# Kernel optimization log

Hardware: AMD Instinct MI355X
Metric: run time of the kernel (lower is better)

## Reference

```python
import jax, jax.numpy as jnp
import numpy as np

DIM = 1024
N_HEADS = 16
HEAD_DIM = DIM // N_HEADS


def setup_inputs() -> dict:
    key = jax.random.key(0)
    ks = jax.random.split(key, 5)
    scale = 1.0 / np.sqrt(DIM)
    x = jax.random.normal(ks[0], (2, 2048, DIM), dtype=jnp.float32)
    W_qkv = jax.random.normal(ks[1], (DIM, 3 * DIM), dtype=jnp.float32) * scale
    b_qkv = jax.random.normal(ks[2], (3 * DIM,), dtype=jnp.float32) * 0.01
    W_proj = jax.random.normal(ks[3], (DIM, DIM), dtype=jnp.float32) * scale
    b_proj = jax.random.normal(ks[4], (DIM,), dtype=jnp.float32) * 0.01
    return {"x": x, "W_qkv": W_qkv, "b_qkv": b_qkv, "W_proj": W_proj, "b_proj": b_proj}


def reference(x, W_qkv, b_qkv, W_proj, b_proj):
    B, T, C = x.shape
    qkv = x @ W_qkv + b_qkv  # [B,T,3C]
    q, k, v = jnp.split(qkv, 3, axis=2)
    # [B,T,C] -> [B,H,T,Dh]
    def heads(y):
        return y.reshape(B, T, N_HEADS, HEAD_DIM).transpose(0, 2, 1, 3)
    q, k, v = heads(q), heads(k), heads(v)
    inv_sqrt_dh = 1.0 / jnp.sqrt(jnp.asarray(HEAD_DIM, dtype=x.dtype))
    attn = jnp.einsum('bhqd,bhkd->bhqk', q, k) * inv_sqrt_dh
    attn = jax.nn.softmax(attn, axis=-1)
    out = jnp.einsum('bhqk,bhkd->bhqd', attn, v)
    out = out.transpose(0, 2, 1, 3).reshape(B, T, C)
    return out @ W_proj + b_proj
```

## Files before the change

kernel.cpp:

```cpp
#include <hip/hip_runtime.h>
#include <hip/hip_bf16.h>
#include <math.h>

using bf16 = __hip_bfloat16;

typedef __bf16 bf16x8 __attribute__((ext_vector_type(8)));
typedef __bf16 bf16x4 __attribute__((ext_vector_type(4)));
typedef float  f32x4  __attribute__((ext_vector_type(4)));
typedef float  f32x16 __attribute__((ext_vector_type(16)));

constexpr int Bb = 2;
constexpr int Ts = 2048;
constexpr int Cc = 1024;
constexpr int Hh = 16;
constexpr int Dh = 64;
constexpr int Mm = Bb * Ts;
constexpr int Nqkv = 3 * Cc;
constexpr int BHTD = Bb * Hh * Ts * Dh;

__device__ __forceinline__
void gll16(const __bf16* g, __bf16* l)
{
    __builtin_amdgcn_global_load_lds(
        (const __attribute__((address_space(1))) unsigned int*)g,
        (__attribute__((address_space(3))) unsigned int*)l,
        16, 0, 0);
}

__global__ __launch_bounds__(256)
void prep_all(const float* __restrict__ x, __bf16* __restrict__ Xb,
              const float* __restrict__ Wq, __bf16* __restrict__ Wqt,
              const float* __restrict__ Wp, __bf16* __restrict__ Wpt)
{
    __shared__ __bf16 tl[64][72];
    const int bid = blockIdx.x;
    const int t = threadIdx.x;

    if (bid < 4096) {
        int i = (bid * 256 + t) * 4;
        float4 v = *(const float4*)(x + i);
        bf16x4 o = { (__bf16)v.x, (__bf16)v.y, (__bf16)v.z, (__bf16)v.w };
        *(bf16x4*)(Xb + i) = o;
        return;
    }
    const float* W; __bf16* Wt; int cols, bx, by;
    if (bid < 4096 + 768) {
        W = Wq; Wt = Wqt; cols = Nqkv;
        bx = (bid - 4096) % 48; by = (bid - 4096) / 48;
    } else {
        W = Wp; Wt = Wpt; cols = Cc;
        bx = (bid - 4864) % 16; by = (bid - 4864) / 16;
    }
    const int c0 = bx * 64;
    const int r0 = by * 64;
    #pragma unroll
    for (int i = 0; i < 4; i++) {
        int e = t + 256 * i;
        int r = e >> 4, c4 = (e & 15) * 4;
        float4 v = *(const float4*)(W + (r0 + r) * cols + c0 + c4);
        bf16x4 o = { (__bf16)v.x, (__bf16)v.y, (__bf16)v.z, (__bf16)v.w };
        *(bf16x4*)&tl[r][c4] = o;
    }
    __syncthreads();
    #pragma unroll
    for (int i = 0; i < 4; i++) {
        int e = t + 256 * i;
        int n = e >> 4, k4 = (e & 15) * 4;
        bf16x4 o = { tl[k4][n], tl[k4 + 1][n], tl[k4 + 2][n], tl[k4 + 3][n] };
        *(bf16x4*)(Wt + (c0 + n) * 1024 + r0 + k4) = o;
    }
}

__device__ __forceinline__
void gemm_core(const __bf16* __restrict__ A, const __bf16* __restrict__ Bt,
               int m0, int n0, int wm, int wn, int quad, int l16, int t,
               f32x4 (&acc)[4][4])
{
    __shared__ __bf16 Al[128][32];
    __shared__ __bf16 Bl[128][32];

    const int wave = t >> 6;
    const int lane = t & 63;
    const int srow = lane >> 2;
    const int scol = (lane & 3) * 8;

    const __bf16* Ag = A  + (size_t)(m0 + wave * 16 + srow) * 1024 + scol;
    const __bf16* Bg = Bt + (size_t)(n0 + wave * 16 + srow) * 1024 + scol;
    __bf16* Al_lo = &Al[wave * 16][0];
    __bf16* Al_hi = &Al[64 + wave * 16][0];
    __bf16* Bl_lo = &Bl[wave * 16][0];
    __bf16* Bl_hi = &Bl[64 + wave * 16][0];

    for (int k0 = 0; k0 < 1024; k0 += 32) {
        gll16(Ag + k0,             Al_lo);
        gll16(Ag + k0 + 64 * 1024, Al_hi);
        gll16(Bg + k0,             Bl_lo);
        gll16(Bg + k0 + 64 * 1024, Bl_hi);
        __syncthreads();
        bf16x8 af[4], bfr[4];
        #pragma unroll
        for (int mt = 0; mt < 4; mt++)
            af[mt] = *(const bf16x8*)&Al[wm * 64 + mt * 16 + l16][quad * 8];
        #pragma unroll
        for (int nt = 0; nt < 4; nt++)
            bfr[nt] = *(const bf16x8*)&Bl[wn * 64 + nt * 16 + l16][quad * 8];
        #pragma unroll
        for (int mt = 0; mt < 4; mt++)
            #pragma unroll
            for (int nt = 0; nt < 4; nt++)
                acc[mt][nt] = __builtin_amdgcn_mfma_f32_16x16x32_bf16(
                    af[mt], bfr[nt], acc[mt][nt], 0, 0, 0);
        __syncthreads();
    }
}

__global__ __launch_bounds__(256)
void qkv_mfma(const __bf16* __restrict__ A, const __bf16* __restrict__ Bt,
              const float* __restrict__ bias, __bf16* __restrict__ qkv)
{
    __shared__ __bf16 ebuf[4][64][72];

    const int t    = threadIdx.x;
    const int wave = t >> 6;
    const int lane = t & 63;
    const int quad = lane >> 4;
    const int l16  = lane & 15;
    const int wm   = wave >> 1, wn = wave & 1;
    const int n0 = blockIdx.x * 128;
    const int m0 = blockIdx.y * 128;

    f32x4 acc[4][4];
    #pragma unroll
    for (int i = 0; i < 4; i++)
        #pragma unroll
        for (int j = 0; j < 4; j++)
            acc[i][j] = f32x4{0.f, 0.f, 0.f, 0.f};

    gemm_core(A, Bt, m0, n0, wm, wn, quad, l16, t, acc);

    const int nw0 = n0 + wn * 64;
    const int which = nw0 >> 10;
    const int h = (nw0 & 1023) >> 6;

    if (which == 2) {
        #pragma unroll
        for (int nt = 0; nt < 4; nt++) {
            int d = nt * 16 + l16;
            float bs = bias[nw0 + nt * 16 + l16];
            #pragma unroll
            for (int mt = 0; mt < 4; mt++) {
                int m = m0 + wm * 64 + mt * 16 + quad * 4;
                int b = m >> 11;
                int tt = m & 2047;
                bf16x4 o = { (__bf16)(acc[mt][nt][0] + bs),
                             (__bf16)(acc[mt][nt][1] + bs),
                             (__bf16)(acc[mt][nt][2] + bs),
                             (__bf16)(acc[mt][nt][3] + bs) };
                *(bf16x4*)&qkv[2 * (size_t)BHTD +
                               (((size_t)(b * 16 + h) * 64 + d) * 2048 + tt)] = o;
            }
        }
    } else {
        #pragma unroll
        for (int nt = 0; nt < 4; nt++) {
            float bs = bias[nw0 + nt * 16 + l16];
            #pragma unroll
            for (int mt = 0; mt < 4; mt++)
                #pragma unroll
                for (int r = 0; r < 4; r++)
                    ebuf[wave][mt * 16 + quad * 4 + r][nt * 16 + l16] =
                        (__bf16)(acc[mt][nt][r] + bs);
        }
        int m = m0 + wm * 64 + lane;
        int b = m >> 11;
        int tt = m & 2047;
        __bf16* dst = &qkv[which * (size_t)BHTD +
                           (((size_t)(b * 16 + h) * 2048 + tt) * 64)];
        #pragma unroll
        for (int c = 0; c < 8; c++)
            *(bf16x8*)(dst + c * 8) = *(const bf16x8*)&ebuf[wave][lane][c * 8];
    }
}

__global__ __launch_bounds__(256)
void proj_mfma(const __bf16* __restrict__ A, const __bf16* __restrict__ Bt,
               const float* __restrict__ bias, float* __restrict__ out)
{
    const int t    = threadIdx.x;
    const int wave = t >> 6;
    const int lane = t & 63;
    const int quad = lane >> 4;
    const int l16  = lane & 15;
    const int wm   = wave >> 1, wn = wave & 1;
    const int n0 = blockIdx.x * 128;
    const int m0 = blockIdx.y * 128;

    f32x4 acc[4][4];
    #pragma unroll
    for (int i = 0; i < 4; i++)
        #pragma unroll
        for (int j = 0; j < 4; j++)
            acc[i][j] = f32x4{0.f, 0.f, 0.f, 0.f};

    gemm_core(A, Bt, m0, n0, wm, wn, quad, l16, t, acc);

    #pragma unroll
    for (int nt = 0; nt < 4; nt++) {
        int n = n0 + wn * 64 + nt * 16 + l16;
        float bs = bias[n];
        #pragma unroll
        for (int mt = 0; mt < 4; mt++) {
            #pragma unroll
            for (int r = 0; r < 4; r++) {
                int m = m0 + wm * 64 + mt * 16 + quad * 4 + r;
                out[m * 1024 + n] = acc[mt][nt][r] + bs;
            }
        }
    }
}

__global__ __launch_bounds__(512, 2)
void attn_mfma(const __bf16* __restrict__ Q, const __bf16* __restrict__ K,
               const __bf16* __restrict__ VT, __bf16* __restrict__ O)
{
    __shared__ __bf16 sK[2][3][64 * 64];
    __shared__ __bf16 sV[2][3][64 * 64];
    __shared__ float  slsum[4][2][64];

    const int t    = threadIdx.x;
    const int wave = t >> 6;
    const int lane = t & 63;
    const int qg   = wave & 3;
    const int kh   = wave >> 2;
    const int c    = lane & 31;
    const int hi   = lane >> 5;
    const int hx   = hi * 16;
    const int sw   = (c & 7) << 4;

    const int blk = blockIdx.x;
    const int bh  = blk & 31;
    const int qc  = blk >> 5;
    const int q0  = qc * 256 + qg * 64;

    const __bf16* Qp = Q  + ((size_t)bh * Ts + q0) * Dh;
    const __bf16* Kp = K  + (size_t)bh * Ts * Dh;
    const __bf16* Vp = VT + (size_t)bh * Dh * Ts;

    const float qscale = 0.125f * 1.44269504088896f;
    bf16x8 qf[2][4];
    #pragma unroll
    for (int qs = 0; qs < 2; qs++)
        #pragma unroll
        for (int ds = 0; ds < 4; ds++) {
            bf16x8 v = *(const bf16x8*)(Qp + (qs * 32 + c) * Dh + ds * 16 + hi * 8);
            #pragma unroll
            for (int i = 0; i < 8; i++) v[i] = (__bf16)(qscale * (float)v[i]);
            qf[qs][ds] = v;
        }

    f32x16 accO[2][2];
    #pragma unroll
    for (int qs = 0; qs < 2; qs++)
        #pragma unroll
        for (int dt = 0; dt < 2; dt++)
            #pragma unroll
            for (int i = 0; i < 16; i++) accO[qs][dt][i] = 0.f;
    float lsum[2] = {0.f, 0.f};

    const f32x16 z16 = {0.f, 0.f, 0.f, 0.f, 0.f, 0.f, 0.f, 0.f,
                        0.f, 0.f, 0.f, 0.f, 0.f, 0.f, 0.f, 0.f};

    const int r0 = qg * 8 + (lane >> 3);
    const int s8 = ((lane & 7) ^ (r0 & 7)) * 8;
    const __bf16* kg0 = Kp + (size_t)(kh * 1024 + r0) * Dh + s8;
    const __bf16* kg1 = kg0 + 32 * Dh;
    const __bf16* vg0 = Vp + (size_t)r0 * Ts + kh * 1024 + s8;
    const __bf16* vg1 = vg0 + (size_t)32 * Ts;

    gll16(kg0, &sK[kh][0][qg * 512]);
    gll16(kg1, &sK[kh][0][2048 + qg * 512]);
    gll16(vg0, &sV[kh][0][qg * 512]);
    gll16(vg1, &sV[kh][0][2048 + qg * 512]);

    for (int j = 0; j < 16; j++) {
        const int p = j % 3;
        if (j < 15) {
            const int pn = (j + 1) % 3;
            gll16(kg0 + (j + 1) * 4096, &sK[kh][pn][qg * 512]);
            gll16(kg1 + (j + 1) * 4096, &sK[kh][pn][2048 + qg * 512]);
            gll16(vg0 + (j + 1) * 64,   &sV[kh][pn][qg * 512]);
            gll16(vg1 + (j + 1) * 64,   &sV[kh][pn][2048 + qg * 512]);
            asm volatile("s_waitcnt vmcnt(4)" ::: "memory");
        } else {
            asm volatile("s_waitcnt vmcnt(0)" ::: "memory");
        }
        __builtin_amdgcn_s_barrier();
        __builtin_amdgcn_sched_barrier(0);

        const char* kb = (const char*)&sK[kh][p][0];
        const char* vb = (const char*)&sV[kh][p][0];

        bf16x8 kf[2][4];
        #pragma unroll
        for (int kt = 0; kt < 2; kt++) {
            const char* rbase = kb + (kt * 32 + c) * 128;
            #pragma unroll
            for (int ds = 0; ds < 4; ds++)
                kf[kt][ds] = *(const bf16x8*)(rbase + ((ds * 32 + hx) ^ sw));
        }

        f32x16 st[2][2];
        __builtin_amdgcn_s_setprio(1);
        #pragma unroll
        for (int kt = 0; kt < 2; kt++)
            #pragma unroll
            for (int qs = 0; qs < 2; qs++)
                st[qs][kt] = __builtin_amdgcn_mfma_f32_32x32x16_bf16(
                    kf[kt][0], qf[qs][0], z16, 0, 0, 0);
        #pragma unroll
        for (int ds = 1; ds < 4; ds++)
            #pragma unroll
            for (int kt = 0; kt < 2; kt++)
                #pragma unroll
                for (int qs = 0; qs < 2; qs++)
                    st[qs][kt] = __builtin_amdgcn_mfma_f32_32x32x16_bf16(
                        kf[kt][ds], qf[qs][ds], st[qs][kt], 0, 0, 0);
        __builtin_amdgcn_s_setprio(0);

        bf16x8 pa[2][4];
        #pragma unroll
        for (int qs = 0; qs < 2; qs++) {
            unsigned pk[2][8];
            #pragma unroll
            for (int kt = 0; kt < 2; kt++) {
                float sum0 = 0.f, sum1 = 0.f;
                #pragma unroll
                for (int r = 0; r < 16; r++) {
                    float pv = __builtin_amdgcn_exp2f(st[qs][kt][r]);
                    st[qs][kt][r] = pv;
                    if (r & 1) sum1 += pv; else sum0 += pv;
                }
                lsum[qs] += sum0 + sum1;
                #pragma unroll
                for (int r2 = 0; r2 < 8; r2++) {
                    unsigned d;
                    asm("v_cvt_pk_bf16_f32 %0, %1, %2"
                        : "=v"(d)
                        : "v"(st[qs][kt][2 * r2]), "v"(st[qs][kt][2 * r2 + 1]));
                    pk[kt][r2] = d;
                }
            }
            #pragma unroll
            for (int s = 0; s < 4; s++) {
                const int kt = s >> 1, r4 = (s & 1) * 4;
                unsigned x0 = pk[kt][r4 + 0], y0 = pk[kt][r4 + 2];
                unsigned x1 = pk[kt][r4 + 1], y1 = pk[kt][r4 + 3];
                asm("v_permlane32_swap_b32 %0, %1" : "+v"(x0), "+v"(y0));
                asm("v_permlane32_swap_b32 %0, %1" : "+v"(x1), "+v"(y1));
                union { unsigned u[4]; bf16x8 b; } pu;
                pu.u[0] = x0; pu.u[1] = x1; pu.u[2] = y0; pu.u[3] = y1;
                pa[qs][s] = pu.b;
            }
        }

        __builtin_amdgcn_s_setprio(1);
        #pragma unroll
        for (int s = 0; s < 4; s++)
            #pragma unroll
            for (int dt = 0; dt < 2; dt++) {
                bf16x8 vf = *(const bf16x8*)(vb + (dt * 32 + c) * 128 +
                                             ((s * 32 + hx) ^ sw));
                #pragma unroll
                for (int qs = 0; qs < 2; qs++)
                    accO[qs][dt] = __builtin_amdgcn_mfma_f32_32x32x16_bf16(
                        pa[qs][s], vf, accO[qs][dt], 0, 0, 0);
            }
        __builtin_amdgcn_s_setprio(0);
    }

    __syncthreads();

    float* pb = (qg < 2) ? (float*)&sK[0][0][0] + qg * 4096
                         : (float*)&sV[0][0][0] + (qg - 2) * 4096;
    if (kh == 1) {
        #pragma unroll
        for (int qs = 0; qs < 2; qs++) {
            #pragma unroll
            for (int dt = 0; dt < 2; dt++)
                #pragma unroll
                for (int r = 0; r < 16; r++)
                    pb[((qs * 2 + dt) << 10) + (r << 6) + lane] = accO[qs][dt][r];
            slsum[qg][qs][lane] = lsum[qs];
        }
    }
    __syncthreads();
    if (kh == 0) {
        #pragma unroll
        for (int qs = 0; qs < 2; qs++) {
            #pragma unroll
            for (int dt = 0; dt < 2; dt++)
                #pragma unroll
                for (int r = 0; r < 16; r++)
                    accO[qs][dt][r] += pb[((qs * 2 + dt) << 10) + (r << 6) + lane];
            lsum[qs] += slsum[qg][qs][lane];
        }

        const int b = bh >> 4, h = bh & 15;
        #pragma unroll
        for (int qs = 0; qs < 2; qs++) {
            float l = lsum[qs] + __shfl_xor(lsum[qs], 32);
            float linv = 1.f / l;
            #pragma unroll
            for (int r = 0; r < 16; r++) {
                const int qrow = (r & 3) + 8 * (r >> 2) + 4 * hi;
                float inv = __shfl(linv, qrow);
                __bf16* Op = O + ((size_t)(b * Ts + q0 + qs * 32 + qrow)) * Cc +
                             h * 64 + c;
                Op[0]  = (__bf16)(accO[qs][0][r] * inv);
                Op[32] = (__bf16)(accO[qs][1][r] * inv);
            }
        }
    }
}

extern "C" void kernel_launch(void* const* d_in, const int* in_sizes, int n_in,
                              void* d_out, int out_size, void* d_ws, size_t ws_size,
                              hipStream_t stream)
{
    (void)in_sizes; (void)n_in; (void)out_size; (void)ws_size;
    const float* x     = (const float*)d_in[0];
    const float* Wqkv  = (const float*)d_in[1];
    const float* bqkv  = (const float*)d_in[2];
    const float* Wproj = (const float*)d_in[3];
    const float* bproj = (const float*)d_in[4];
    float* out = (float*)d_out;

    __bf16* ws   = (__bf16*)d_ws;
    __bf16* Qw   = ws;
    __bf16* XbAO = ws + 3 * (size_t)BHTD;
    __bf16* Wqt  = XbAO + (size_t)Mm * Cc;
    __bf16* Wpt  = Wqt + (size_t)Nqkv * Cc;

    prep_all<<<dim3(5120), 256, 0, stream>>>(x, XbAO, Wqkv, Wqt, Wproj, Wpt);
    qkv_mfma<<<dim3(Nqkv / 128, Mm / 128), 256, 0, stream>>>(XbAO, Wqt, bqkv, Qw);
    attn_mfma<<<dim3(256), 512, 0, stream>>>(
        Qw, Qw + BHTD, Qw + 2 * (size_t)BHTD, XbAO);
    proj_mfma<<<dim3(Cc / 128, Mm / 128), 256, 0, stream>>>(XbAO, Wpt, bproj, out);
}
```

Before: 189.1 us.

## Halve attention and projection tiles to double block counts and occupancy

The attention kernel now gives each wave 32 query rows instead of 64 and launches 512 blocks instead of 256. It drops from triple to double buffering of K/V in shared memory and fuses the score, exp and PV steps per 32-key subtile, which cuts register and LDS use so four blocks can fit per CU. The projection GEMM switches to 64-row M tiles through a templated gemm_core, doubling its grid to fill more CUs. In exchange, K/V tiles are reloaded twice as often per query, and the double buffer leaves less prefetch slack because of the full vmcnt(0) wait at the top of each iteration.

```diff
diff --git a/kernel.cpp b/kernel.cpp
--- a/kernel.cpp
+++ b/kernel.cpp
@@ -71,14 +71,16 @@
     }
 }
 
+template<int BM>
 __device__ __forceinline__
 void gemm_core(const __bf16* __restrict__ A, const __bf16* __restrict__ Bt,
                int m0, int n0, int wm, int wn, int quad, int l16, int t,
                f32x4 (&acc)[4][4])
 {
-    __shared__ __bf16 Al[128][32];
+    __shared__ __bf16 Al[BM][32];
     __shared__ __bf16 Bl[128][32];
 
+    constexpr int MT = BM / 32;
     const int wave = t >> 6;
     const int lane = t & 63;
     const int srow = lane >> 2;
@@ -87,25 +89,27 @@
     const __bf16* Ag = A  + (size_t)(m0 + wave * 16 + srow) * 1024 + scol;
     const __bf16* Bg = Bt + (size_t)(n0 + wave * 16 + srow) * 1024 + scol;
     __bf16* Al_lo = &Al[wave * 16][0];
-    __bf16* Al_hi = &Al[64 + wave * 16][0];
     __bf16* Bl_lo = &Bl[wave * 16][0];
     __bf16* Bl_hi = &Bl[64 + wave * 16][0];
 
     for (int k0 = 0; k0 < 1024; k0 += 32) {
-        gll16(Ag + k0,             Al_lo);
-        gll16(Ag + k0 + 64 * 1024, Al_hi);
+        gll16(Ag + k0, Al_lo);
+        if constexpr (BM == 128) {
+            __bf16* Al_hi = &Al[64 + wave * 16][0];
+            gll16(Ag + k0 + 64 * 1024, Al_hi);
+        }
         gll16(Bg + k0,             Bl_lo);
         gll16(Bg + k0 + 64 * 1024, Bl_hi);
         __syncthreads();
-        bf16x8 af[4], bfr[4];
-        #pragma unroll
-        for (int mt = 0; mt < 4; mt++)
-            af[mt] = *(const bf16x8*)&Al[wm * 64 + mt * 16 + l16][quad * 8];
+        bf16x8 af[MT], bfr[4];
+        #pragma unroll
+        for (int mt = 0; mt < MT; mt++)
+            af[mt] = *(const bf16x8*)&Al[wm * (BM / 2) + mt * 16 + l16][quad * 8];
         #pragma unroll
         for (int nt = 0; nt < 4; nt++)
             bfr[nt] = *(const bf16x8*)&Bl[wn * 64 + nt * 16 + l16][quad * 8];
         #pragma unroll
-        for (int mt = 0; mt < 4; mt++)
+        for (int mt = 0; mt < MT; mt++)
             #pragma unroll
             for (int nt = 0; nt < 4; nt++)
                 acc[mt][nt] = __builtin_amdgcn_mfma_f32_16x16x32_bf16(
@@ -136,7 +140,7 @@
         for (int j = 0; j < 4; j++)
             acc[i][j] = f32x4{0.f, 0.f, 0.f, 0.f};
 
-    gemm_core(A, Bt, m0, n0, wm, wn, quad, l16, t, acc);
+    gemm_core<128>(A, Bt, m0, n0, wm, wn, quad, l16, t, acc);
 
     const int nw0 = n0 + wn * 64;
     const int which = nw0 >> 10;
@@ -193,7 +197,7 @@
     const int l16  = lane & 15;
     const int wm   = wave >> 1, wn = wave & 1;
     const int n0 = blockIdx.x * 128;
-    const int m0 = blockIdx.y * 128;
+    const int m0 = blockIdx.y * 64;
 
     f32x4 acc[4][4];
     #pragma unroll
@@ -202,30 +206,30 @@
         for (int j = 0; j < 4; j++)
             acc[i][j] = f32x4{0.f, 0.f, 0.f, 0.f};
 
-    gemm_core(A, Bt, m0, n0, wm, wn, quad, l16, t, acc);
+    gemm_core<64>(A, Bt, m0, n0, wm, wn, quad, l16, t, acc);
 
     #pragma unroll
     for (int nt = 0; nt < 4; nt++) {
         int n = n0 + wn * 64 + nt * 16 + l16;
         float bs = bias[n];
         #pragma unroll
-        for (int mt = 0; mt < 4; mt++) {
+        for (int mt = 0; mt < 2; mt++) {
             #pragma unroll
             for (int r = 0; r < 4; r++) {
-                int m = m0 + wm * 64 + mt * 16 + quad * 4 + r;
+                int m = m0 + wm * 32 + mt * 16 + quad * 4 + r;
                 out[m * 1024 + n] = acc[mt][nt][r] + bs;
             }
         }
     }
 }
 
-__global__ __launch_bounds__(512, 2)
+__global__ __launch_bounds__(512, 4)
 void attn_mfma(const __bf16* __restrict__ Q, const __bf16* __restrict__ K,
                const __bf16* __restrict__ VT, __bf16* __restrict__ O)
 {
-    __shared__ __bf16 sK[2][3][64 * 64];
-    __shared__ __bf16 sV[2][3][64 * 64];
-    __shared__ float  slsum[4][2][64];
+    __shared__ __bf16 sK[2][2][64 * 64];
+    __shared__ __bf16 sV[2][2][64 * 64];
+    __shared__ float  slsum[4][64];
 
     const int t    = threadIdx.x;
     const int wave = t >> 6;
@@ -240,32 +244,28 @@
     const int blk = blockIdx.x;
     const int bh  = blk & 31;
     const int qc  = blk >> 5;
-    const int q0  = qc * 256 + qg * 64;
+    const int q0  = qc * 128 + qg * 32;
 
     const __bf16* Qp = Q  + ((size_t)bh * Ts + q0) * Dh;
     const __bf16* Kp = K  + (size_t)bh * Ts * Dh;
     const __bf16* Vp = VT + (size_t)bh * Dh * Ts;
 
     const float qscale = 0.125f * 1.44269504088896f;
-    bf16x8 qf[2][4];
-    #pragma unroll
-    for (int qs = 0; qs < 2; qs++)
-        #pragma unroll
-        for (int ds = 0; ds < 4; ds++) {
-            bf16x8 v = *(const bf16x8*)(Qp + (qs * 32 + c) * Dh + ds * 16 + hi * 8);
-            #pragma unroll
-            for (int i = 0; i < 8; i++) v[i] = (__bf16)(qscale * (float)v[i]);
-            qf[qs][ds] = v;
-        }
-
-    f32x16 accO[2][2];
-    #pragma unroll
-    for (int qs = 0; qs < 2; qs++)
-        #pragma unroll
-        for (int dt = 0; dt < 2; dt++)
-            #pragma unroll
-            for (int i = 0; i < 16; i++) accO[qs][dt][i] = 0.f;
-    float lsum[2] = {0.f, 0.f};
+    bf16x8 qf[4];
+    #pragma unroll
+    for (int ds = 0; ds < 4; ds++) {
+        bf16x8 v = *(const bf16x8*)(Qp + c * Dh + ds * 16 + hi * 8);
+        #pragma unroll
+        for (int i = 0; i < 8; i++) v[i] = (__bf16)(qscale * (float)v[i]);
+        qf[ds] = v;
+    }
+
+    f32x16 accO[2];
+    #pragma unroll
+    for (int dt = 0; dt < 2; dt++)
+        #pragma unroll
+        for (int i = 0; i < 16; i++) accO[dt][i] = 0.f;
+    float lsum = 0.f;
 
     const f32x16 z16 = {0.f, 0.f, 0.f, 0.f, 0.f, 0.f, 0.f, 0.f,
                         0.f, 0.f, 0.f, 0.f, 0.f, 0.f, 0.f, 0.f};
@@ -283,142 +283,108 @@
     gll16(vg1, &sV[kh][0][2048 + qg * 512]);
 
     for (int j = 0; j < 16; j++) {
-        const int p = j % 3;
+        const int p = j & 1;
+        asm volatile("s_waitcnt vmcnt(0)" ::: "memory");
+        __builtin_amdgcn_s_barrier();
+        __builtin_amdgcn_sched_barrier(0);
         if (j < 15) {
-            const int pn = (j + 1) % 3;
+            const int pn = p ^ 1;
             gll16(kg0 + (j + 1) * 4096, &sK[kh][pn][qg * 512]);
             gll16(kg1 + (j + 1) * 4096, &sK[kh][pn][2048 + qg * 512]);
             gll16(vg0 + (j + 1) * 64,   &sV[kh][pn][qg * 512]);
             gll16(vg1 + (j + 1) * 64,   &sV[kh][pn][2048 + qg * 512]);
-            asm volatile("s_waitcnt vmcnt(4)" ::: "memory");
-        } else {
-            asm volatile("s_waitcnt vmcnt(0)" ::: "memory");
-        }
-        __builtin_amdgcn_s_barrier();
-        __builtin_amdgcn_sched_barrier(0);
-
+        }
         const char* kb = (const char*)&sK[kh][p][0];
         const char* vb = (const char*)&sV[kh][p][0];
 
-        bf16x8 kf[2][4];
         #pragma unroll
         for (int kt = 0; kt < 2; kt++) {
             const char* rbase = kb + (kt * 32 + c) * 128;
-            #pragma unroll
-            for (int ds = 0; ds < 4; ds++)
-                kf[kt][ds] = *(const bf16x8*)(rbase + ((ds * 32 + hx) ^ sw));
-        }
-
-        f32x16 st[2][2];
-        __builtin_amdgcn_s_setprio(1);
-        #pragma unroll
-        for (int kt = 0; kt < 2; kt++)
-            #pragma unroll
-            for (int qs = 0; qs < 2; qs++)
-                st[qs][kt] = __builtin_amdgcn_mfma_f32_32x32x16_bf16(
-                    kf[kt][0], qf[qs][0], z16, 0, 0, 0);
-        #pragma unroll
-        for (int ds = 1; ds < 4; ds++)
-            #pragma unroll
-            for (int kt = 0; kt < 2; kt++)
+            bf16x8 kf0 = *(const bf16x8*)(rbase + ((0 * 32 + hx) ^ sw));
+            bf16x8 kf1 = *(const bf16x8*)(rbase + ((1 * 32 + hx) ^ sw));
+            f32x16 st;
+            __builtin_amdgcn_s_setprio(1);
+            st = __builtin_amdgcn_mfma_f32_32x32x16_bf16(kf0, qf[0], z16, 0, 0, 0);
+            st = __builtin_amdgcn_mfma_f32_32x32x16_bf16(kf1, qf[1], st, 0, 0, 0);
+            __builtin_amdgcn_s_setprio(0);
+            bf16x8 kf2 = *(const bf16x8*)(rbase + ((2 * 32 + hx) ^ sw));
+            bf16x8 kf3 = *(const bf16x8*)(rbase + ((3 * 32 + hx) ^ sw));
+            __builtin_amdgcn_s_setprio(1);
+            st = __builtin_amdgcn_mfma_f32_32x32x16_bf16(kf2, qf[2], st, 0, 0, 0);
+            st = __builtin_amdgcn_mfma_f32_32x32x16_bf16(kf3, qf[3], st, 0, 0, 0);
+            __builtin_amdgcn_s_setprio(0);
+
+            float sum0 = 0.f, sum1 = 0.f;
+            #pragma unroll
+            for (int r = 0; r < 16; r++) {
+                float pv = __builtin_amdgcn_exp2f(st[r]);
+                st[r] = pv;
+                if (r & 1) sum1 += pv; else sum0 += pv;
+            }
+            lsum += sum0 + sum1;
+
+            #pragma unroll
+            for (int s2 = 0; s2 < 2; s2++) {
+                unsigned pk0, pk1, pk2, pk3;
+                const int r4 = s2 * 8;
+                asm("v_cvt_pk_bf16_f32 %0, %1, %2"
+                    : "=v"(pk0) : "v"(st[r4 + 0]), "v"(st[r4 + 1]));
+                asm("v_cvt_pk_bf16_f32 %0, %1, %2"
+                    : "=v"(pk1) : "v"(st[r4 + 2]), "v"(st[r4 + 3]));
+                asm("v_cvt_pk_bf16_f32 %0, %1, %2"
+                    : "=v"(pk2) : "v"(st[r4 + 4]), "v"(st[r4 + 5]));
+                asm("v_cvt_pk_bf16_f32 %0, %1, %2"
+                    : "=v"(pk3) : "v"(st[r4 + 6]), "v"(st[r4 + 7]));
+                asm("v_permlane32_swap_b32 %0, %1" : "+v"(pk0), "+v"(pk2));
+                asm("v_permlane32_swap_b32 %0, %1" : "+v"(pk1), "+v"(pk3));
+                union { unsigned u[4]; bf16x8 b; } pu;
+                pu.u[0] = pk0; pu.u[1] = pk1; pu.u[2] = pk2; pu.u[3] = pk3;
+                const bf16x8 pa = pu.b;
+
+                const int so = (kt * 2 + s2) * 32;
+                __builtin_amdgcn_s_setprio(1);
                 #pragma unroll
-                for (int qs = 0; qs < 2; qs++)
-                    st[qs][kt] = __builtin_amdgcn_mfma_f32_32x32x16_bf16(
-                        kf[kt][ds], qf[qs][ds], st[qs][kt], 0, 0, 0);
-        __builtin_amdgcn_s_setprio(0);
-
-        bf16x8 pa[2][4];
-        #pragma unroll
-        for (int qs = 0; qs < 2; qs++) {
-            unsigned pk[2][8];
-            #pragma unroll
-            for (int kt = 0; kt < 2; kt++) {
-                float sum0 = 0.f, sum1 = 0.f;
-                #pragma unroll
-                for (int r = 0; r < 16; r++) {
-                    float pv = __builtin_amdgcn_exp2f(st[qs][kt][r]);
-                    st[qs][kt][r] = pv;
-                    if (r & 1) sum1 += pv; else sum0 += pv;
+                for (int dt = 0; dt < 2; dt++) {
+                    bf16x8 vf = *(const bf16x8*)(vb + (dt * 32 + c) * 128 +
+                                                 ((so + hx) ^ sw));
+                    accO[dt] = __builtin_amdgcn_mfma_f32_32x32x16_bf16(
+                        pa, vf, accO[dt], 0, 0, 0);
                 }
-                lsum[qs] += sum0 + sum1;
-                #pragma unroll
-                for (int r2 = 0; r2 < 8; r2++) {
-                    unsigned d;
-                    asm("v_cvt_pk_bf16_f32 %0, %1, %2"
-                        : "=v"(d)
-                        : "v"(st[qs][kt][2 * r2]), "v"(st[qs][kt][2 * r2 + 1]));
-                    pk[kt][r2] = d;
-                }
+                __builtin_amdgcn_s_setprio(0);
             }
-            #pragma unroll
-            for (int s = 0; s < 4; s++) {
-                const int kt = s >> 1, r4 = (s & 1) * 4;
-                unsigned x0 = pk[kt][r4 + 0], y0 = pk[kt][r4 + 2];
-                unsigned x1 = pk[kt][r4 + 1], y1 = pk[kt][r4 + 3];
-                asm("v_permlane32_swap_b32 %0, %1" : "+v"(x0), "+v"(y0));
-                asm("v_permlane32_swap_b32 %0, %1" : "+v"(x1), "+v"(y1));
-                union { unsigned u[4]; bf16x8 b; } pu;
-                pu.u[0] = x0; pu.u[1] = x1; pu.u[2] = y0; pu.u[3] = y1;
-                pa[qs][s] = pu.b;
-            }
-        }
-
-        __builtin_amdgcn_s_setprio(1);
-        #pragma unroll
-        for (int s = 0; s < 4; s++)
-            #pragma unroll
-            for (int dt = 0; dt < 2; dt++) {
-                bf16x8 vf = *(const bf16x8*)(vb + (dt * 32 + c) * 128 +
-                                             ((s * 32 + hx) ^ sw));
-                #pragma unroll
-                for (int qs = 0; qs < 2; qs++)
-                    accO[qs][dt] = __builtin_amdgcn_mfma_f32_32x32x16_bf16(
-                        pa[qs][s], vf, accO[qs][dt], 0, 0, 0);
-            }
-        __builtin_amdgcn_s_setprio(0);
+        }
     }
 
     __syncthreads();
 
-    float* pb = (qg < 2) ? (float*)&sK[0][0][0] + qg * 4096
-                         : (float*)&sV[0][0][0] + (qg - 2) * 4096;
+    float* pb = (float*)&sK[0][0][0] + qg * 2048;
     if (kh == 1) {
         #pragma unroll
-        for (int qs = 0; qs < 2; qs++) {
-            #pragma unroll
-            for (int dt = 0; dt < 2; dt++)
-                #pragma unroll
-                for (int r = 0; r < 16; r++)
-                    pb[((qs * 2 + dt) << 10) + (r << 6) + lane] = accO[qs][dt][r];
-            slsum[qg][qs][lane] = lsum[qs];
-        }
+        for (int dt = 0; dt < 2; dt++)
+            #pragma unroll
+            for (int r = 0; r < 16; r++)
+                pb[(dt << 10) + (r << 6) + lane] = accO[dt][r];
+        slsum[qg][lane] = lsum;
     }
     __syncthreads();
     if (kh == 0) {
         #pragma unroll
-        for (int qs = 0; qs < 2; qs++) {
-            #pragma unroll
-            for (int dt = 0; dt < 2; dt++)
-                #pragma unroll
-                for (int r = 0; r < 16; r++)
-                    accO[qs][dt][r] += pb[((qs * 2 + dt) << 10) + (r << 6) + lane];
-            lsum[qs] += slsum[qg][qs][lane];
-        }
+        for (int dt = 0; dt < 2; dt++)
+            #pragma unroll
+            for (int r = 0; r < 16; r++)
+                accO[dt][r] += pb[(dt << 10) + (r << 6) + lane];
+        lsum += slsum[qg][lane];
 
         const int b = bh >> 4, h = bh & 15;
-        #pragma unroll
-        for (int qs = 0; qs < 2; qs++) {
-            float l = lsum[qs] + __shfl_xor(lsum[qs], 32);
-            float linv = 1.f / l;
-            #pragma unroll
-            for (int r = 0; r < 16; r++) {
-                const int qrow = (r & 3) + 8 * (r >> 2) + 4 * hi;
-                float inv = __shfl(linv, qrow);
-                __bf16* Op = O + ((size_t)(b * Ts + q0 + qs * 32 + qrow)) * Cc +
-                             h * 64 + c;
-                Op[0]  = (__bf16)(accO[qs][0][r] * inv);
-                Op[32] = (__bf16)(accO[qs][1][r] * inv);
-            }
+        float l = lsum + __shfl_xor(lsum, 32);
+        float linv = 1.f / l;
+        #pragma unroll
+        for (int r = 0; r < 16; r++) {
+            const int qrow = (r & 3) + 8 * (r >> 2) + 4 * hi;
+            float inv = __shfl(linv, qrow);
+            __bf16* Op = O + ((size_t)(b * Ts + q0 + qrow)) * Cc + h * 64 + c;
+            Op[0]  = (__bf16)(accO[0][r] * inv);
+            Op[32] = (__bf16)(accO[1][r] * inv);
         }
     }
 }
@@ -443,7 +409,7 @@
 
     prep_all<<<dim3(5120), 256, 0, stream>>>(x, XbAO, Wqkv, Wqt, Wproj, Wpt);
     qkv_mfma<<<dim3(Nqkv / 128, Mm / 128), 256, 0, stream>>>(XbAO, Wqt, bqkv, Qw);
-    attn_mfma<<<dim3(256), 512, 0, stream>>>(
+    attn_mfma<<<dim3(512), 512, 0, stream>>>(
         Qw, Qw + BHTD, Qw + 2 * (size_t)BHTD, XbAO);
-    proj_mfma<<<dim3(Cc / 128, Mm / 128), 256, 0, stream>>>(XbAO, Wpt, bproj, out);
-}
+    proj_mfma<<<dim3(Cc / 128, Mm / 64), 256, 0, stream>>>(XbAO, Wpt, bproj, out);
+}
```

Measured after the change: 182.1 us. 3.7% less time.

## Split attention KV range across four wave groups and halve proj GEMM M tile

Applied to the files above, without the earlier changes.

The attention kernel grows from 512 to 1024 threads per block, splitting the key/value sequence four ways instead of two. It swaps the triple-buffered pipeline with a wait-for-all prefetch for a double-buffered one, and merges the partial results with a two-stage tree through shared memory. The projection GEMM moves to a 64-row M tile via a templated gemm_core, doubling its grid to 512 blocks for better CU fill on the small output. The trade-offs are weaker load/compute overlap in attention (vmcnt(0) every iteration), an extra barrier-based reduction, and more register pressure under the 1024-thread launch bound.

```diff
diff --git a/kernel.cpp b/kernel.cpp
--- a/kernel.cpp
+++ b/kernel.cpp
@@ -71,14 +71,16 @@
     }
 }
 
+template<int BM>
 __device__ __forceinline__
 void gemm_core(const __bf16* __restrict__ A, const __bf16* __restrict__ Bt,
                int m0, int n0, int wm, int wn, int quad, int l16, int t,
                f32x4 (&acc)[4][4])
 {
-    __shared__ __bf16 Al[128][32];
+    __shared__ __bf16 Al[BM][32];
     __shared__ __bf16 Bl[128][32];
 
+    constexpr int MT = BM / 32;
     const int wave = t >> 6;
     const int lane = t & 63;
     const int srow = lane >> 2;
@@ -87,25 +89,27 @@
     const __bf16* Ag = A  + (size_t)(m0 + wave * 16 + srow) * 1024 + scol;
     const __bf16* Bg = Bt + (size_t)(n0 + wave * 16 + srow) * 1024 + scol;
     __bf16* Al_lo = &Al[wave * 16][0];
-    __bf16* Al_hi = &Al[64 + wave * 16][0];
     __bf16* Bl_lo = &Bl[wave * 16][0];
     __bf16* Bl_hi = &Bl[64 + wave * 16][0];
 
     for (int k0 = 0; k0 < 1024; k0 += 32) {
-        gll16(Ag + k0,             Al_lo);
-        gll16(Ag + k0 + 64 * 1024, Al_hi);
+        gll16(Ag + k0, Al_lo);
+        if constexpr (BM == 128) {
+            __bf16* Al_hi = &Al[64 + wave * 16][0];
+            gll16(Ag + k0 + 64 * 1024, Al_hi);
+        }
         gll16(Bg + k0,             Bl_lo);
         gll16(Bg + k0 + 64 * 1024, Bl_hi);
         __syncthreads();
-        bf16x8 af[4], bfr[4];
-        #pragma unroll
-        for (int mt = 0; mt < 4; mt++)
-            af[mt] = *(const bf16x8*)&Al[wm * 64 + mt * 16 + l16][quad * 8];
+        bf16x8 af[MT], bfr[4];
+        #pragma unroll
+        for (int mt = 0; mt < MT; mt++)
+            af[mt] = *(const bf16x8*)&Al[wm * (BM / 2) + mt * 16 + l16][quad * 8];
         #pragma unroll
         for (int nt = 0; nt < 4; nt++)
             bfr[nt] = *(const bf16x8*)&Bl[wn * 64 + nt * 16 + l16][quad * 8];
         #pragma unroll
-        for (int mt = 0; mt < 4; mt++)
+        for (int mt = 0; mt < MT; mt++)
             #pragma unroll
             for (int nt = 0; nt < 4; nt++)
                 acc[mt][nt] = __builtin_amdgcn_mfma_f32_16x16x32_bf16(
@@ -136,7 +140,7 @@
         for (int j = 0; j < 4; j++)
             acc[i][j] = f32x4{0.f, 0.f, 0.f, 0.f};
 
-    gemm_core(A, Bt, m0, n0, wm, wn, quad, l16, t, acc);
+    gemm_core<128>(A, Bt, m0, n0, wm, wn, quad, l16, t, acc);
 
     const int nw0 = n0 + wn * 64;
     const int which = nw0 >> 10;
@@ -193,7 +197,7 @@
     const int l16  = lane & 15;
     const int wm   = wave >> 1, wn = wave & 1;
     const int n0 = blockIdx.x * 128;
-    const int m0 = blockIdx.y * 128;
+    const int m0 = blockIdx.y * 64;
 
     f32x4 acc[4][4];
     #pragma unroll
@@ -202,30 +206,30 @@
         for (int j = 0; j < 4; j++)
             acc[i][j] = f32x4{0.f, 0.f, 0.f, 0.f};
 
-    gemm_core(A, Bt, m0, n0, wm, wn, quad, l16, t, acc);
+    gemm_core<64>(A, Bt, m0, n0, wm, wn, quad, l16, t, acc);
 
     #pragma unroll
     for (int nt = 0; nt < 4; nt++) {
         int n = n0 + wn * 64 + nt * 16 + l16;
         float bs = bias[n];
         #pragma unroll
-        for (int mt = 0; mt < 4; mt++) {
+        for (int mt = 0; mt < 2; mt++) {
             #pragma unroll
             for (int r = 0; r < 4; r++) {
-                int m = m0 + wm * 64 + mt * 16 + quad * 4 + r;
+                int m = m0 + wm * 32 + mt * 16 + quad * 4 + r;
                 out[m * 1024 + n] = acc[mt][nt][r] + bs;
             }
         }
     }
 }
 
-__global__ __launch_bounds__(512, 2)
+__global__ __launch_bounds__(1024, 4)
 void attn_mfma(const __bf16* __restrict__ Q, const __bf16* __restrict__ K,
                const __bf16* __restrict__ VT, __bf16* __restrict__ O)
 {
-    __shared__ __bf16 sK[2][3][64 * 64];
-    __shared__ __bf16 sV[2][3][64 * 64];
-    __shared__ float  slsum[4][2][64];
+    __shared__ __bf16 sK[4][2][64 * 64];
+    __shared__ __bf16 sV[4][2][64 * 64];
+    __shared__ float  sLs[4][4][2][64];
 
     const int t    = threadIdx.x;
     const int wave = t >> 6;
@@ -272,9 +276,9 @@
 
     const int r0 = qg * 8 + (lane >> 3);
     const int s8 = ((lane & 7) ^ (r0 & 7)) * 8;
-    const __bf16* kg0 = Kp + (size_t)(kh * 1024 + r0) * Dh + s8;
+    const __bf16* kg0 = Kp + (size_t)(kh * 512 + r0) * Dh + s8;
     const __bf16* kg1 = kg0 + 32 * Dh;
-    const __bf16* vg0 = Vp + (size_t)r0 * Ts + kh * 1024 + s8;
+    const __bf16* vg0 = Vp + (size_t)r0 * Ts + kh * 512 + s8;
     const __bf16* vg1 = vg0 + (size_t)32 * Ts;
 
     gll16(kg0, &sK[kh][0][qg * 512]);
@@ -282,21 +286,18 @@
     gll16(vg0, &sV[kh][0][qg * 512]);
     gll16(vg1, &sV[kh][0][2048 + qg * 512]);
 
-    for (int j = 0; j < 16; j++) {
-        const int p = j % 3;
-        if (j < 15) {
-            const int pn = (j + 1) % 3;
+    for (int j = 0; j < 8; j++) {
+        const int p = j & 1;
+        asm volatile("s_waitcnt vmcnt(0)" ::: "memory");
+        __builtin_amdgcn_s_barrier();
+        __builtin_amdgcn_sched_barrier(0);
+        if (j < 7) {
+            const int pn = p ^ 1;
             gll16(kg0 + (j + 1) * 4096, &sK[kh][pn][qg * 512]);
             gll16(kg1 + (j + 1) * 4096, &sK[kh][pn][2048 + qg * 512]);
             gll16(vg0 + (j + 1) * 64,   &sV[kh][pn][qg * 512]);
             gll16(vg1 + (j + 1) * 64,   &sV[kh][pn][2048 + qg * 512]);
-            asm volatile("s_waitcnt vmcnt(4)" ::: "memory");
-        } else {
-            asm volatile("s_waitcnt vmcnt(0)" ::: "memory");
-        }
-        __builtin_amdgcn_s_barrier();
-        __builtin_amdgcn_sched_barrier(0);
-
+        }
         const char* kb = (const char*)&sK[kh][p][0];
         const char* vb = (const char*)&sV[kh][p][0];
 
@@ -380,29 +381,59 @@
 
     __syncthreads();
 
-    float* pb = (qg < 2) ? (float*)&sK[0][0][0] + qg * 4096
-                         : (float*)&sV[0][0][0] + (qg - 2) * 4096;
-    if (kh == 1) {
+    float* baseK = (float*)&sK[0][0][0];
+    float* baseV = (float*)&sV[0][0][0];
+
+    if (kh >= 2) {
+        float* pb = (kh == 2 ? baseK : baseV) + qg * 4096;
         #pragma unroll
         for (int qs = 0; qs < 2; qs++) {
             #pragma unroll
             for (int dt = 0; dt < 2; dt++)
                 #pragma unroll
                 for (int r = 0; r < 16; r++)
-                    pb[((qs * 2 + dt) << 10) + (r << 6) + lane] = accO[qs][dt][r];
-            slsum[qg][qs][lane] = lsum[qs];
+                    pb[qs * 2048 + dt * 1024 + (r << 6) + lane] = accO[qs][dt][r];
+            sLs[kh][qg][qs][lane] = lsum[qs];
         }
     }
     __syncthreads();
     if (kh == 0) {
+        const float* pb = baseK + qg * 4096;
         #pragma unroll
         for (int qs = 0; qs < 2; qs++) {
             #pragma unroll
             for (int dt = 0; dt < 2; dt++)
                 #pragma unroll
                 for (int r = 0; r < 16; r++)
-                    accO[qs][dt][r] += pb[((qs * 2 + dt) << 10) + (r << 6) + lane];
-            lsum[qs] += slsum[qg][qs][lane];
+                    accO[qs][dt][r] += pb[qs * 2048 + dt * 1024 + (r << 6) + lane];
+            lsum[qs] += sLs[2][qg][qs][lane];
+        }
+    } else if (kh == 1) {
+        float* pb = baseV + qg * 4096;
+        #pragma unroll
+        for (int qs = 0; qs < 2; qs++) {
+            #pragma unroll
+            for (int dt = 0; dt < 2; dt++)
+                #pragma unroll
+                for (int r = 0; r < 16; r++) {
+                    float v = accO[qs][dt][r] + pb[qs * 2048 + dt * 1024 + (r << 6) + lane];
+                    accO[qs][dt][r] = v;
+                    pb[qs * 2048 + dt * 1024 + (r << 6) + lane] = v;
+                }
+            sLs[1][qg][qs][lane] = lsum[qs] + sLs[3][qg][qs][lane];
+        }
+    }
+    __syncthreads();
+    if (kh == 0) {
+        const float* pb = baseV + qg * 4096;
+        #pragma unroll
+        for (int qs = 0; qs < 2; qs++) {
+            #pragma unroll
+            for (int dt = 0; dt < 2; dt++)
+                #pragma unroll
+                for (int r = 0; r < 16; r++)
+                    accO[qs][dt][r] += pb[qs * 2048 + dt * 1024 + (r << 6) + lane];
+            lsum[qs] += sLs[1][qg][qs][lane];
         }
 
         const int b = bh >> 4, h = bh & 15;
@@ -443,7 +474,7 @@
 
     prep_all<<<dim3(5120), 256, 0, stream>>>(x, XbAO, Wqkv, Wqt, Wproj, Wpt);
     qkv_mfma<<<dim3(Nqkv / 128, Mm / 128), 256, 0, stream>>>(XbAO, Wqt, bqkv, Qw);
-    attn_mfma<<<dim3(256), 512, 0, stream>>>(
+    attn_mfma<<<dim3(256), 1024, 0, stream>>>(
         Qw, Qw + BHTD, Qw + 2 * (size_t)BHTD, XbAO);
-    proj_mfma<<<dim3(Cc / 128, Mm / 128), 256, 0, stream>>>(XbAO, Wpt, bproj, out);
-}
+    proj_mfma<<<dim3(Cc / 128, Mm / 64), 256, 0, stream>>>(XbAO, Wpt, bproj, out);
+}
```

New measurement: 355.3 us. 87.9% more time.
